# Performance work log

Hardware: AMD Instinct MI355X
Metric: run time of the kernel (lower is better)

The kernel has to match this reference:

```python
import jax, jax.numpy as jnp
import numpy as np

N_ATOMS = 10000
N_EDGES = 250000
F_DIM = 128
N_RBF = 20
CUTOFF = 5.0
N_INT = 3
EPS = 1e-8


def setup_inputs() -> dict:
    key = jax.random.key(0)
    ks = jax.random.split(key, 16)
    inp = {}
    inp["atomic_numbers"] = jax.random.randint(ks[0], (N_ATOMS,), 1, 101)
    # positions in a 5 Angstrom box so many pairs lie inside the cutoff
    inp["R"] = jax.random.uniform(ks[1], (N_ATOMS, 3), dtype=jnp.float32) * 5.0
    idx_i = jnp.sort(jax.random.randint(ks[2], (N_EDGES,), 0, N_ATOMS))
    # ensure idx_j != idx_i so d_ij > 0
    idx_j = (idx_i + 1 + jax.random.randint(ks[3], (N_EDGES,), 0, N_ATOMS - 1)) % N_ATOMS
    inp["idx_i"] = idx_i
    inp["idx_j"] = idx_j
    inp["offsets"] = jnp.zeros((N_EDGES, 3), dtype=jnp.float32)

    def w(k, shape):
        fan_in = shape[-2]
        return jax.random.normal(k, shape, dtype=jnp.float32) / np.sqrt(fan_in).astype(np.float32)

    inp["emb"] = jax.random.normal(ks[4], (101, F_DIM), dtype=jnp.float32)
    inp["filt_W"] = w(ks[5], (N_RBF, 3 * F_DIM))
    inp["filt_b"] = jax.random.normal(ks[6], (3 * F_DIM,), dtype=jnp.float32) * 0.01
    inp["int_W1"] = w(ks[7], (N_INT, F_DIM, F_DIM))
    inp["int_b1"] = jnp.zeros((N_INT, 1, F_DIM), dtype=jnp.float32)
    inp["int_W2"] = w(ks[8], (N_INT, F_DIM, 3 * F_DIM))
    inp["int_b2"] = jnp.zeros((N_INT, 1, 3 * F_DIM), dtype=jnp.float32)
    inp["mix_Wmu"] = w(ks[9], (N_INT, F_DIM, 2 * F_DIM))
    inp["mix_W1"] = w(ks[10], (N_INT, 2 * F_DIM, F_DIM))
    inp["mix_b1"] = jnp.zeros((N_INT, 1, F_DIM), dtype=jnp.float32)
    inp["mix_W2"] = w(ks[11], (N_INT, F_DIM, 3 * F_DIM))
    inp["mix_b2"] = jnp.zeros((N_INT, 1, 3 * F_DIM), dtype=jnp.float32)
    return inp


def painn_forward(atomic_numbers, idx_i, idx_j, R, offsets, emb, filt_W, filt_b,
                  int_W1, int_b1, int_W2, int_b2,
                  mix_Wmu, mix_W1, mix_b1, mix_W2, mix_b2):
    n_atoms = atomic_numbers.shape[0]
    # geometry
    r_ij = R[idx_j] - R[idx_i] + offsets                      # [E,3]
    d_ij = jnp.linalg.norm(r_ij, axis=1, keepdims=True)       # [E,1]
    dir_ij = r_ij / d_ij                                      # [E,3]
    # Gaussian radial basis + cosine cutoff (schnetpack defaults)
    centers = jnp.linspace(0.0, CUTOFF, N_RBF, dtype=jnp.float32)
    coeff = -0.5 / (centers[1] - centers[0]) ** 2
    phi = jnp.exp(coeff * (d_ij[..., None] - centers) ** 2)   # [E,1,N_RBF]
    fcut = 0.5 * (jnp.cos(d_ij * (jnp.pi / CUTOFF)) + 1.0) * (d_ij < CUTOFF)  # [E,1]
    Wij = (phi @ filt_W + filt_b) * fcut[..., None]           # [E,1,3F] (shared filters)

    q = emb[atomic_numbers][:, None, :]                       # [N,1,F]
    mu = jnp.zeros((n_atoms, 3, F_DIM), dtype=q.dtype)        # [N,3,F]

    for i in range(N_INT):
        # ---- interaction (equivariant message passing) ----
        x = jax.nn.silu(q @ int_W1[i] + int_b1[i]) @ int_W2[i] + int_b2[i]  # [N,1,3F]
        xj = x[idx_j]                                          # [E,1,3F]
        muj = mu[idx_j]                                        # [E,3,F]
        xw = Wij * xj                                          # [E,1,3F]
        dq, dmuR, dmumu = jnp.split(xw, 3, axis=-1)            # each [E,1,F]
        dq = jax.ops.segment_sum(dq, idx_i, num_segments=n_atoms)          # [N,1,F]
        dmu = dmuR * dir_ij[..., None] + dmumu * muj           # [E,3,F]
        dmu = jax.ops.segment_sum(dmu, idx_i, num_segments=n_atoms)        # [N,3,F]
        q = q + dq
        mu = mu + dmu
        # ---- mixing (intra-atomic) ----
        mu_mix = mu @ mix_Wmu[i]                               # [N,3,2F]
        mu_V, mu_W = jnp.split(mu_mix, 2, axis=-1)             # [N,3,F] each
        mu_Vn = jnp.sqrt(jnp.sum(mu_V ** 2, axis=-2, keepdims=True) + EPS)  # [N,1,F]
        ctx = jnp.concatenate([q, mu_Vn], axis=-1)             # [N,1,2F]
        xm = jax.nn.silu(ctx @ mix_W1[i] + mix_b1[i]) @ mix_W2[i] + mix_b2[i]  # [N,1,3F]
        dq_intra, dmu_intra, dqmu_intra = jnp.split(xm, 3, axis=-1)
        dmu_intra = dmu_intra * mu_W                           # [N,3,F]
        dqmu_intra = dqmu_intra * jnp.sum(mu_V * mu_W, axis=1, keepdims=True)  # [N,1,F]
        q = q + dq_intra + dqmu_intra
        mu = mu + dmu_intra

    return q.squeeze(1), mu                                    # [N,F], [N,3,F]


def reference(atomic_numbers, R, idx_i, idx_j, offsets, emb, filt_W, filt_b,
              int_W1, int_b1, int_W2, int_b2,
              mix_Wmu, mix_W1, mix_b1, mix_W2, mix_b2):
    return painn_forward(atomic_numbers, idx_i, idx_j, R, offsets, emb, filt_W, filt_b,
                         int_W1, int_b1, int_W2, int_b2,
                         mix_Wmu, mix_W1, mix_b1, mix_W2, mix_b2)
```

## Files before the change

kernel.cpp:

```cpp
#include <hip/hip_runtime.h>
#include <math.h>

#define NA 10000
#define NE 250000
#define FD 128
#define NRBF 20
#define RCUT 5.0f

typedef _Float16 h16;
typedef __attribute__((ext_vector_type(8))) _Float16 half8;
typedef __attribute__((ext_vector_type(4))) float f32x4;

static __device__ __forceinline__ half8 f32x8_to_h8(const float* p) {
    float4 a = *(const float4*)p;
    float4 b = *(const float4*)(p + 4);
    half8 r;
    r[0] = (h16)a.x; r[1] = (h16)a.y; r[2] = (h16)a.z; r[3] = (h16)a.w;
    r[4] = (h16)b.x; r[5] = (h16)b.y; r[6] = (h16)b.z; r[7] = (h16)b.w;
    return r;
}
static __device__ __forceinline__ float silu(float v) {
    return v / (1.f + expf(-v));
}

__global__ __launch_bounds__(256) void setup_kernel(
    const float* __restrict__ R, const int* __restrict__ idx_i,
    const int* __restrict__ idx_j, const float* __restrict__ offsets,
    float* __restrict__ dir, h16* __restrict__ ph, int* __restrict__ row_start,
    const float* __restrict__ int_W1, const float* __restrict__ int_W2,
    const float* __restrict__ mix_Wmu, const float* __restrict__ mix_W1,
    const float* __restrict__ mix_W2,
    h16* __restrict__ W1t, h16* __restrict__ W2t, h16* __restrict__ WmuT,
    h16* __restrict__ mW1t, h16* __restrict__ mW2t,
    const float* __restrict__ filt_W, const float* __restrict__ filt_b,
    h16* __restrict__ fwt)
{
    const int b = blockIdx.x;
    if (b < 977) {
        int e = b * 256 + threadIdx.x;
        if (e >= NE) return;
        int i = idx_i[e], j = idx_j[e];
        float rx = R[j * 3 + 0] - R[i * 3 + 0] + offsets[e * 3 + 0];
        float ry = R[j * 3 + 1] - R[i * 3 + 1] + offsets[e * 3 + 1];
        float rz = R[j * 3 + 2] - R[i * 3 + 2] + offsets[e * 3 + 2];
        float d = sqrtf(rx * rx + ry * ry + rz * rz);
        float inv = 1.f / d;
        float fcut = 0.f;
        if (d < RCUT) fcut = 0.5f * (cosf(d * (3.14159265358979323846f / RCUT)) + 1.f);
        *(float4*)&dir[(size_t)e * 4] = make_float4(rx * inv, ry * inv, rz * inv, 0.f);
        h16* pp = ph + (size_t)e * 32;
        const float delta = RCUT / 19.f;
        const float coeff = -0.5f / (delta * delta);
#pragma unroll
        for (int r = 0; r < NRBF; ++r) {
            float dc = d - (float)r * delta;
            pp[r] = (h16)(expf(coeff * dc * dc) * fcut);
        }
        pp[20] = (h16)fcut;
#pragma unroll
        for (int r = 21; r < 32; ++r) pp[r] = (h16)0.f;
    } else if (b < 1017) {
        int n = (b - 977) * 256 + threadIdx.x;
        if (n > NA) return;
        int lo = 0, hi = NE;
        while (lo < hi) {
            int mid = (lo + hi) >> 1;
            if (idx_i[mid] < n) lo = mid + 1; else hi = mid;
        }
        row_start[n] = lo;
    } else {
        int idx = (b - 1017) * 256 + threadIdx.x;
        if (idx < 49152) {
            int bt = idx >> 14, rem = idx & 16383;
            int nn = rem >> 7, kk = rem & 127;
            W1t[idx] = (h16)int_W1[(size_t)bt * 16384 + kk * 128 + nn];
        } else if ((idx -= 49152) < 147456) {
            int bt = idx / 49152, rem = idx - bt * 49152;
            int nn = rem >> 7, kk = rem & 127;
            W2t[idx] = (h16)int_W2[(size_t)bt * 49152 + kk * 384 + nn];
        } else if ((idx -= 147456) < 98304) {
            int bt = idx >> 15, rem = idx & 32767;
            int nn = rem >> 7, kk = rem & 127;
            WmuT[idx] = (h16)mix_Wmu[(size_t)bt * 32768 + kk * 256 + nn];
        } else if ((idx -= 98304) < 98304) {
            int bt = idx >> 15, rem = idx & 32767;
            int nn = rem >> 8, kk = rem & 255;
            mW1t[idx] = (h16)mix_W1[(size_t)bt * 32768 + kk * 128 + nn];
        } else if ((idx -= 98304) < 147456) {
            int bt = idx / 49152, rem = idx - bt * 49152;
            int nn = rem >> 7, kk = rem & 127;
            mW2t[idx] = (h16)mix_W2[(size_t)bt * 49152 + kk * 384 + nn];
        } else if ((idx -= 147456) < 12288) {
            int nn = idx >> 5, kk = idx & 31;
            float v = 0.f;
            if (kk < 20) v = filt_W[kk * 384 + nn];
            else if (kk == 20) v = filt_b[nn];
            fwt[idx] = (h16)v;
        }
    }
}

__global__ __launch_bounds__(256) void intmlp0_kernel(
    const int* __restrict__ Z, const float* __restrict__ emb, float* __restrict__ q,
    const h16* __restrict__ W1t, const float* __restrict__ b1,
    const h16* __restrict__ W2t, const float* __restrict__ b2, h16* __restrict__ x16)
{
    __shared__ h16 Hs[16 * 136];
    const int tid = threadIdx.x;
    const int wave = tid >> 6, lane = tid & 63;
    const int ar = lane & 15, kg = lane >> 4;
    const size_t row0 = (size_t)blockIdx.x * 16;

    {
        int a = tid >> 4, f0 = (tid & 15) * 8;
        const float* src = emb + (size_t)Z[row0 + a] * 128 + f0;
        float4 v0 = *(const float4*)src;
        float4 v1 = *(const float4*)(src + 4);
        *(float4*)&q[(row0 + a) * 128 + f0] = v0;
        *(float4*)&q[(row0 + a) * 128 + f0 + 4] = v1;
    }
    const int zr = Z[row0 + ar];
    f32x4 a1[2] = {};
    for (int ks = 0; ks < 128; ks += 32) {
        int k = ks + kg * 8;
        half8 af = f32x8_to_h8(emb + (size_t)zr * 128 + k);
#pragma unroll
        for (int tt = 0; tt < 2; ++tt) {
            int t = wave * 2 + tt;
            half8 bf = *(const half8*)&W1t[(size_t)(t * 16 + ar) * 128 + k];
            a1[tt] = __builtin_amdgcn_mfma_f32_16x16x32_f16(af, bf, a1[tt], 0, 0, 0);
        }
    }
#pragma unroll
    for (int tt = 0; tt < 2; ++tt) {
        int col = (wave * 2 + tt) * 16 + ar;
        float bb = b1[col];
#pragma unroll
        for (int r = 0; r < 4; ++r)
            Hs[(kg * 4 + r) * 136 + col] = (h16)silu(a1[tt][r] + bb);
    }
    __syncthreads();
    f32x4 a2[6] = {};
    for (int ks = 0; ks < 128; ks += 32) {
        int k = ks + kg * 8;
        half8 af = *(const half8*)&Hs[ar * 136 + k];
#pragma unroll
        for (int tt = 0; tt < 6; ++tt) {
            int t = wave * 6 + tt;
            half8 bf = *(const half8*)&W2t[(size_t)(t * 16 + ar) * 128 + k];
            a2[tt] = __builtin_amdgcn_mfma_f32_16x16x32_f16(af, bf, a2[tt], 0, 0, 0);
        }
    }
#pragma unroll
    for (int tt = 0; tt < 6; ++tt) {
        int col = (wave * 6 + tt) * 16 + ar;
        float bb = b2[col];
#pragma unroll
        for (int r = 0; r < 4; ++r)
            x16[(row0 + kg * 4 + r) * 384 + col] = (h16)(a2[tt][r] + bb);
    }
}

template<bool HAS_MU>
__global__ __launch_bounds__(128) void edge_kernel(
    const float* __restrict__ dir, const h16* __restrict__ ph,
    const h16* __restrict__ fwt,
    const int* __restrict__ row_start, const int* __restrict__ idx_j,
    const h16* __restrict__ x16, const h16* __restrict__ mu16p,
    const float* __restrict__ mup, float* __restrict__ mun,
    h16* __restrict__ mu16n, float* __restrict__ q)
{
    const int n = blockIdx.x, tid = threadIdx.x;
    const int wave = tid >> 6, lane = tid & 63;
    const int c = lane & 15, kg = lane >> 4;
    const int e0 = row_start[n], e1 = row_start[n + 1];

    float adq[4] = {}, am0[4] = {}, am1[4] = {}, am2[4] = {};

    for (int eg = e0; eg < e1; eg += 16) {
        int ea = eg + c; if (ea >= e1) ea = e1 - 1;
        half8 af = *(const half8*)&ph[(size_t)ea * 32 + kg * 8];
        f32x4 cw0[4], cw1[4], cw2[4];
#pragma unroll
        for (int tf = 0; tf < 4; ++tf) {
            f32x4 z = {0.f, 0.f, 0.f, 0.f};
            half8 b0 = *(const half8*)&fwt[(size_t)(((4 * wave + tf) * 16 + c)) * 32 + kg * 8];
            cw0[tf] = __builtin_amdgcn_mfma_f32_16x16x32_f16(af, b0, z, 0, 0, 0);
            half8 b1 = *(const half8*)&fwt[(size_t)(((8 + 4 * wave + tf) * 16 + c)) * 32 + kg * 8];
            cw1[tf] = __builtin_amdgcn_mfma_f32_16x16x32_f16(af, b1, z, 0, 0, 0);
            if (HAS_MU) {
                half8 b2 = *(const half8*)&fwt[(size_t)(((16 + 4 * wave + tf) * 16 + c)) * 32 + kg * 8];
                cw2[tf] = __builtin_amdgcn_mfma_f32_16x16x32_f16(af, b2, z, 0, 0, 0);
            } else {
                cw2[tf] = z;
            }
        }
#pragma unroll
        for (int r = 0; r < 4; ++r) {
            int e = eg + kg * 4 + r;
            if (e < e1) {
                int j = idx_j[e];
                float4 g = *(const float4*)&dir[(size_t)e * 4];
                const h16* xb = x16 + (size_t)j * 384;
#pragma unroll
                for (int tf = 0; tf < 4; ++tf) {
                    int fo = wave * 64 + tf * 16 + c;
                    float x0 = (float)xb[fo];
                    float x1 = (float)xb[128 + fo];
                    adq[tf] = fmaf(cw0[tf][r], x0, adq[tf]);
                    float t1 = cw1[tf][r] * x1;
                    if (HAS_MU) {
                        const h16* mb = mu16p + (size_t)j * 384;
                        float x2 = (float)xb[256 + fo];
                        float t2 = cw2[tf][r] * x2;
                        am0[tf] += t1 * g.x + t2 * (float)mb[fo];
                        am1[tf] += t1 * g.y + t2 * (float)mb[128 + fo];
                        am2[tf] += t1 * g.z + t2 * (float)mb[256 + fo];
                    } else {
                        am0[tf] = fmaf(t1, g.x, am0[tf]);
                        am1[tf] = fmaf(t1, g.y, am1[tf]);
                        am2[tf] = fmaf(t1, g.z, am2[tf]);
                    }
                }
            }
        }
    }

#pragma unroll
    for (int tf = 0; tf < 4; ++tf) {
        adq[tf] += __shfl_xor(adq[tf], 16); adq[tf] += __shfl_xor(adq[tf], 32);
        am0[tf] += __shfl_xor(am0[tf], 16); am0[tf] += __shfl_xor(am0[tf], 32);
        am1[tf] += __shfl_xor(am1[tf], 16); am1[tf] += __shfl_xor(am1[tf], 32);
        am2[tf] += __shfl_xor(am2[tf], 16); am2[tf] += __shfl_xor(am2[tf], 32);
    }
    if (kg == 0) {
        size_t b = (size_t)n * 384;
#pragma unroll
        for (int tf = 0; tf < 4; ++tf) {
            int fo = wave * 64 + tf * 16 + c;
            q[(size_t)n * 128 + fo] += adq[tf];
            float m0 = (HAS_MU ? mup[b + fo] : 0.f) + am0[tf];
            float m1 = (HAS_MU ? mup[b + 128 + fo] : 0.f) + am1[tf];
            float m2 = (HAS_MU ? mup[b + 256 + fo] : 0.f) + am2[tf];
            mun[b + fo] = m0; mun[b + 128 + fo] = m1; mun[b + 256 + fo] = m2;
            mu16n[b + fo] = (h16)m0; mu16n[b + 128 + fo] = (h16)m1; mu16n[b + 256 + fo] = (h16)m2;
        }
    }
}

__global__ __launch_bounds__(256) void mixint_kernel(
    const h16* __restrict__ mu16n, const h16* __restrict__ WmuT,
    const h16* __restrict__ W1t, const float* __restrict__ b1,
    const h16* __restrict__ W2t, const float* __restrict__ b2,
    float* __restrict__ q, float* __restrict__ mu, h16* __restrict__ mu16w,
    const h16* __restrict__ nW1t, const float* __restrict__ nb1,
    const h16* __restrict__ nW2t, const float* __restrict__ nb2,
    h16* __restrict__ x16)
{
    __shared__ h16 MM[48 * 264];
    __shared__ h16 CT[16 * 264];
    __shared__ h16 Hs[16 * 136];
    __shared__ h16 XM[16 * 392];
    const int tid = threadIdx.x;
    const int wave = tid >> 6, lane = tid & 63;
    const int ar = lane & 15, kg = lane >> 4;
    const size_t row0 = (size_t)blockIdx.x * 16;

    {
        f32x4 acc[3][4] = {};
        int aloc[3], dloc[3];
#pragma unroll
        for (int rt = 0; rt < 3; ++rt) {
            int rr = rt * 16 + ar;
            aloc[rt] = rr / 3;
            dloc[rt] = rr - 3 * aloc[rt];
        }
        for (int ks = 0; ks < 128; ks += 32) {
            int k = ks + kg * 8;
            half8 afr[3];
#pragma unroll
            for (int rt = 0; rt < 3; ++rt)
                afr[rt] = *(const half8*)&mu16n[(row0 + aloc[rt]) * 384 + dloc[rt] * 128 + k];
#pragma unroll
            for (int ct = 0; ct < 4; ++ct) {
                int cc = wave * 4 + ct;
                half8 bf = *(const half8*)&WmuT[(size_t)(cc * 16 + ar) * 128 + k];
#pragma unroll
                for (int rt = 0; rt < 3; ++rt)
                    acc[rt][ct] = __builtin_amdgcn_mfma_f32_16x16x32_f16(afr[rt], bf, acc[rt][ct], 0, 0, 0);
            }
        }
#pragma unroll
        for (int rt = 0; rt < 3; ++rt)
#pragma unroll
            for (int ct = 0; ct < 4; ++ct) {
                int col = (wave * 4 + ct) * 16 + ar;
#pragma unroll
                for (int r = 0; r < 4; ++r)
                    MM[(rt * 16 + kg * 4 + r) * 264 + col] = (h16)acc[rt][ct][r];
            }
    }
    __syncthreads();

    {
        int a = tid >> 4, fi = (tid & 15) * 8;
        const float* qp = q + (row0 + a) * 128 + fi;
        float4 q0 = *(const float4*)qp;
        float4 q1 = *(const float4*)(qp + 4);
        float qv[8] = {q0.x, q0.y, q0.z, q0.w, q1.x, q1.y, q1.z, q1.w};
#pragma unroll
        for (int jj = 0; jj < 8; ++jj) {
            int ff = fi + jj;
            float v0 = (float)MM[(a * 3 + 0) * 264 + ff];
            float v1 = (float)MM[(a * 3 + 1) * 264 + ff];
            float v2 = (float)MM[(a * 3 + 2) * 264 + ff];
            CT[a * 264 + 128 + ff] = (h16)sqrtf(v0 * v0 + v1 * v1 + v2 * v2 + 1e-8f);
            CT[a * 264 + ff] = (h16)qv[jj];
        }
    }
    __syncthreads();

    {
        f32x4 a1[2] = {};
        for (int ks = 0; ks < 256; ks += 32) {
            int k = ks + kg * 8;
            half8 af = *(const half8*)&CT[ar * 264 + k];
#pragma unroll
            for (int tt = 0; tt < 2; ++tt) {
                int t = wave * 2 + tt;
                half8 bf = *(const half8*)&W1t[(size_t)(t * 16 + ar) * 256 + k];
                a1[tt] = __builtin_amdgcn_mfma_f32_16x16x32_f16(af, bf, a1[tt], 0, 0, 0);
            }
        }
#pragma unroll
        for (int tt = 0; tt < 2; ++tt) {
            int col = (wave * 2 + tt) * 16 + ar;
            float bb = b1[col];
#pragma unroll
            for (int r = 0; r < 4; ++r)
                Hs[(kg * 4 + r) * 136 + col] = (h16)silu(a1[tt][r] + bb);
        }
    }
    __syncthreads();

    {
        f32x4 a2[6] = {};
        for (int ks = 0; ks < 128; ks += 32) {
            int k = ks + kg * 8;
            half8 af = *(const half8*)&Hs[ar * 136 + k];
#pragma unroll
            for (int tt = 0; tt < 6; ++tt) {
                int t = wave * 6 + tt;
                half8 bf = *(const half8*)&W2t[(size_t)(t * 16 + ar) * 128 + k];
                a2[tt] = __builtin_amdgcn_mfma_f32_16x16x32_f16(af, bf, a2[tt], 0, 0, 0);
            }
        }
#pragma unroll
        for (int tt = 0; tt < 6; ++tt) {
            int col = (wave * 6 + tt) * 16 + ar;
            float bb = b2[col];
#pragma unroll
            for (int r = 0; r < 4; ++r)
                XM[(kg * 4 + r) * 392 + col] = (h16)(a2[tt][r] + bb);
        }
    }
    __syncthreads();

    {
        int a = tid >> 4, fi = (tid & 15) * 8;
        size_t n = row0 + a;
#pragma unroll
        for (int jj = 0; jj < 8; ++jj) {
            int ff = fi + jj;
            float dq  = (float)XM[a * 392 + ff];
            float dm  = (float)XM[a * 392 + 128 + ff];
            float dqm = (float)XM[a * 392 + 256 + ff];
            float v0 = (float)MM[(a * 3 + 0) * 264 + ff], w0 = (float)MM[(a * 3 + 0) * 264 + 128 + ff];
            float v1 = (float)MM[(a * 3 + 1) * 264 + ff], w1 = (float)MM[(a * 3 + 1) * 264 + 128 + ff];
            float v2 = (float)MM[(a * 3 + 2) * 264 + ff], w2 = (float)MM[(a * 3 + 2) * 264 + 128 + ff];
            float sv = v0 * w0 + v1 * w1 + v2 * w2;
            float qn = q[n * 128 + ff] + dq + dqm * sv;
            q[n * 128 + ff] = qn;
            CT[a * 264 + ff] = (h16)qn;
            size_t b = n * 384 + ff;
            float m0 = mu[b] + dm * w0;
            float m1 = mu[b + 128] + dm * w1;
            float m2 = mu[b + 256] + dm * w2;
            mu[b] = m0; mu[b + 128] = m1; mu[b + 256] = m2;
            mu16w[b] = (h16)m0; mu16w[b + 128] = (h16)m1; mu16w[b + 256] = (h16)m2;
        }
    }
    if (!nW1t) return;
    __syncthreads();

    {
        f32x4 a1[2] = {};
        for (int ks = 0; ks < 128; ks += 32) {
            int k = ks + kg * 8;
            half8 af = *(const half8*)&CT[ar * 264 + k];
#pragma unroll
            for (int tt = 0; tt < 2; ++tt) {
                int t = wave * 2 + tt;
                half8 bf = *(const half8*)&nW1t[(size_t)(t * 16 + ar) * 128 + k];
                a1[tt] = __builtin_amdgcn_mfma_f32_16x16x32_f16(af, bf, a1[tt], 0, 0, 0);
            }
        }
#pragma unroll
        for (int tt = 0; tt < 2; ++tt) {
            int col = (wave * 2 + tt) * 16 + ar;
            float bb = nb1[col];
#pragma unroll
            for (int r = 0; r < 4; ++r)
                Hs[(kg * 4 + r) * 136 + col] = (h16)silu(a1[tt][r] + bb);
        }
        __syncthreads();
        f32x4 a2[6] = {};
        for (int ks = 0; ks < 128; ks += 32) {
            int k = ks + kg * 8;
            half8 af = *(const half8*)&Hs[ar * 136 + k];
#pragma unroll
            for (int tt = 0; tt < 6; ++tt) {
                int t = wave * 6 + tt;
                half8 bf = *(const half8*)&nW2t[(size_t)(t * 16 + ar) * 128 + k];
                a2[tt] = __builtin_amdgcn_mfma_f32_16x16x32_f16(af, bf, a2[tt], 0, 0, 0);
            }
        }
#pragma unroll
        for (int tt = 0; tt < 6; ++tt) {
            int col = (wave * 6 + tt) * 16 + ar;
            float bb = nb2[col];
#pragma unroll
            for (int r = 0; r < 4; ++r)
                x16[(row0 + kg * 4 + r) * 384 + col] = (h16)(a2[tt][r] + bb);
        }
    }
}

extern "C" void kernel_launch(void* const* d_in, const int* in_sizes, int n_in,
                              void* d_out, int out_size, void* d_ws, size_t ws_size,
                              hipStream_t stream)
{
    const int*   Z       = (const int*)d_in[0];
    const float* R       = (const float*)d_in[1];
    const int*   idx_i   = (const int*)d_in[2];
    const int*   idx_j   = (const int*)d_in[3];
    const float* offsets = (const float*)d_in[4];
    const float* emb     = (const float*)d_in[5];
    const float* filt_W  = (const float*)d_in[6];
    const float* filt_b  = (const float*)d_in[7];
    const float* int_W1  = (const float*)d_in[8];
    const float* int_b1  = (const float*)d_in[9];
    const float* int_W2  = (const float*)d_in[10];
    const float* int_b2  = (const float*)d_in[11];
    const float* mix_Wmu = (const float*)d_in[12];
    const float* mix_W1  = (const float*)d_in[13];
    const float* mix_b1  = (const float*)d_in[14];
    const float* mix_W2  = (const float*)d_in[15];
    const float* mix_b2  = (const float*)d_in[16];

    float* q_out  = (float*)d_out;
    float* mu_out = (float*)d_out + (size_t)NA * FD;

    char* base = (char*)d_ws;
    size_t o = 0;
    auto alloc = [&](size_t bytes) -> void* {
        void* p = base + o;
        o += (bytes + 255) & ~(size_t)255;
        return p;
    };
    float* dir    = (float*)alloc((size_t)NE * 4 * 4);
    h16*   ph     = (h16*)alloc((size_t)NE * 32 * 2);
    h16*   x16    = (h16*)alloc((size_t)NA * 384 * 2);
    h16*   mu16a  = (h16*)alloc((size_t)NA * 384 * 2);
    h16*   mu16b  = (h16*)alloc((size_t)NA * 384 * 2);
    float* mu_ws  = (float*)alloc((size_t)NA * 384 * 4);
    h16*   W1t    = (h16*)alloc((size_t)3 * 128 * 128 * 2);
    h16*   W2t    = (h16*)alloc((size_t)3 * 384 * 128 * 2);
    h16*   WmuT   = (h16*)alloc((size_t)3 * 256 * 128 * 2);
    h16*   mW1t   = (h16*)alloc((size_t)3 * 128 * 256 * 2);
    h16*   mW2t   = (h16*)alloc((size_t)3 * 384 * 128 * 2);
    h16*   fwt    = (h16*)alloc((size_t)384 * 32 * 2);
    int*   row_st = (int*)alloc((size_t)(NA + 1) * 4);

    setup_kernel<<<3177, 256, 0, stream>>>(R, idx_i, idx_j, offsets, dir, ph, row_st,
                                           int_W1, int_W2, mix_Wmu, mix_W1, mix_W2,
                                           W1t, W2t, WmuT, mW1t, mW2t,
                                           filt_W, filt_b, fwt);

    intmlp0_kernel<<<NA / 16, 256, 0, stream>>>(Z, emb, q_out,
                                                W1t, int_b1, W2t, int_b2, x16);
    edge_kernel<false><<<NA, 128, 0, stream>>>(dir, ph, fwt, row_st, idx_j,
                                               x16, nullptr, nullptr, mu_out, mu16b, q_out);
    mixint_kernel<<<NA / 16, 256, 0, stream>>>(
        mu16b, WmuT, mW1t, mix_b1, mW2t, mix_b2, q_out, mu_out, mu16b,
        W1t + 16384, int_b1 + 128, W2t + 49152, int_b2 + 384, x16);

    edge_kernel<true><<<NA, 128, 0, stream>>>(dir, ph, fwt, row_st, idx_j,
                                              x16, mu16b, mu_out, mu_ws, mu16a, q_out);
    mixint_kernel<<<NA / 16, 256, 0, stream>>>(
        mu16a, WmuT + 32768, mW1t + 32768, mix_b1 + 128, mW2t + 49152, mix_b2 + 384,
        q_out, mu_ws, mu16a,
        W1t + 32768, int_b1 + 256, W2t + 98304, int_b2 + 768, x16);

    edge_kernel<true><<<NA, 128, 0, stream>>>(dir, ph, fwt, row_st, idx_j,
                                              x16, mu16a, mu_ws, mu_out, mu16b, q_out);
    mixint_kernel<<<NA / 16, 256, 0, stream>>>(
        mu16b, WmuT + 65536, mW1t + 65536, mix_b1 + 256, mW2t + 98304, mix_b2 + 768,
        q_out, mu_out, mu16b,
        nullptr, nullptr, nullptr, nullptr, nullptr);
}
```

Baseline: 474.9 us.

## Transpose edge MFMA so lanes own edges and gather contiguous half4 features

The edge kernel now uses four waves per atom, each owning 32 features. The filter weights become the register-resident A operand, loaded once per block, and the per-edge RBF values become the B operand. Each lane now handles one edge and four consecutive features, so gathers from x16 and mu16 become vectorized half4 loads instead of scalar half loads. The next edge group's ph, idx_j and dir are prefetched one iteration ahead. The cost is a longer 4-step shuffle reduction across the 16 edge lanes, and 256-thread blocks that may lower occupancy.

```diff
diff --git a/kernel.cpp b/kernel.cpp
--- a/kernel.cpp
+++ b/kernel.cpp
@@ -9,6 +9,7 @@
 
 typedef _Float16 h16;
 typedef __attribute__((ext_vector_type(8))) _Float16 half8;
+typedef __attribute__((ext_vector_type(4))) _Float16 half4;
 typedef __attribute__((ext_vector_type(4))) float f32x4;
 
 static __device__ __forceinline__ half8 f32x8_to_h8(const float* p) {
@@ -162,7 +163,7 @@
 }
 
 template<bool HAS_MU>
-__global__ __launch_bounds__(128) void edge_kernel(
+__global__ __launch_bounds__(256) void edge_kernel(
     const float* __restrict__ dir, const h16* __restrict__ ph,
     const h16* __restrict__ fwt,
     const int* __restrict__ row_start, const int* __restrict__ idx_j,
@@ -174,52 +175,74 @@
     const int wave = tid >> 6, lane = tid & 63;
     const int c = lane & 15, kg = lane >> 4;
     const int e0 = row_start[n], e1 = row_start[n + 1];
-
-    float adq[4] = {}, am0[4] = {}, am1[4] = {}, am2[4] = {};
-
-    for (int eg = e0; eg < e1; eg += 16) {
-        int ea = eg + c; if (ea >= e1) ea = e1 - 1;
-        half8 af = *(const half8*)&ph[(size_t)ea * 32 + kg * 8];
-        f32x4 cw0[4], cw1[4], cw2[4];
-#pragma unroll
-        for (int tf = 0; tf < 4; ++tf) {
+    const int f0 = wave * 32;
+
+    half8 afq[2], afr[2], afm[2];
+#pragma unroll
+    for (int t = 0; t < 2; ++t) {
+        int fr = f0 + 16 * t + c;
+        afq[t] = *(const half8*)&fwt[(size_t)fr * 32 + kg * 8];
+        afr[t] = *(const half8*)&fwt[(size_t)(128 + fr) * 32 + kg * 8];
+        if (HAS_MU)
+            afm[t] = *(const half8*)&fwt[(size_t)(256 + fr) * 32 + kg * 8];
+    }
+
+    f32x4 adq[2] = {}, am0[2] = {}, am1[2] = {}, am2[2] = {};
+
+    if (e0 < e1) {
+        int ec = e0 + c; int ecl = ec < e1 ? ec : e1 - 1;
+        half8 bf = *(const half8*)&ph[(size_t)ecl * 32 + kg * 8];
+        int j = idx_j[ecl];
+        float4 g = *(const float4*)&dir[(size_t)ecl * 4];
+
+        for (int eg = e0; eg < e1; eg += 16) {
+            half8 bf_c = bf; int j_c = j; float4 g_c = g;
+            bool v_c = (eg + c) < e1;
+            int eg2 = eg + 16;
+            if (eg2 < e1) {
+                int e2 = eg2 + c; int ecl2 = e2 < e1 ? e2 : e1 - 1;
+                bf = *(const half8*)&ph[(size_t)ecl2 * 32 + kg * 8];
+                j = idx_j[ecl2];
+                g = *(const float4*)&dir[(size_t)ecl2 * 4];
+            }
             f32x4 z = {0.f, 0.f, 0.f, 0.f};
-            half8 b0 = *(const half8*)&fwt[(size_t)(((4 * wave + tf) * 16 + c)) * 32 + kg * 8];
-            cw0[tf] = __builtin_amdgcn_mfma_f32_16x16x32_f16(af, b0, z, 0, 0, 0);
-            half8 b1 = *(const half8*)&fwt[(size_t)(((8 + 4 * wave + tf) * 16 + c)) * 32 + kg * 8];
-            cw1[tf] = __builtin_amdgcn_mfma_f32_16x16x32_f16(af, b1, z, 0, 0, 0);
-            if (HAS_MU) {
-                half8 b2 = *(const half8*)&fwt[(size_t)(((16 + 4 * wave + tf) * 16 + c)) * 32 + kg * 8];
-                cw2[tf] = __builtin_amdgcn_mfma_f32_16x16x32_f16(af, b2, z, 0, 0, 0);
-            } else {
-                cw2[tf] = z;
-            }
-        }
-#pragma unroll
-        for (int r = 0; r < 4; ++r) {
-            int e = eg + kg * 4 + r;
-            if (e < e1) {
-                int j = idx_j[e];
-                float4 g = *(const float4*)&dir[(size_t)e * 4];
-                const h16* xb = x16 + (size_t)j * 384;
-#pragma unroll
-                for (int tf = 0; tf < 4; ++tf) {
-                    int fo = wave * 64 + tf * 16 + c;
-                    float x0 = (float)xb[fo];
-                    float x1 = (float)xb[128 + fo];
-                    adq[tf] = fmaf(cw0[tf][r], x0, adq[tf]);
-                    float t1 = cw1[tf][r] * x1;
+            f32x4 cwq[2], cwr[2], cwm[2];
+#pragma unroll
+            for (int t = 0; t < 2; ++t) {
+                cwq[t] = __builtin_amdgcn_mfma_f32_16x16x32_f16(afq[t], bf_c, z, 0, 0, 0);
+                cwr[t] = __builtin_amdgcn_mfma_f32_16x16x32_f16(afr[t], bf_c, z, 0, 0, 0);
+                if (HAS_MU)
+                    cwm[t] = __builtin_amdgcn_mfma_f32_16x16x32_f16(afm[t], bf_c, z, 0, 0, 0);
+            }
+            if (v_c) {
+                const h16* xb = x16 + (size_t)j_c * 384;
+#pragma unroll
+                for (int t = 0; t < 2; ++t) {
+                    int fb = f0 + 16 * t + kg * 4;
+                    half4 x0 = *(const half4*)&xb[fb];
+                    half4 x1 = *(const half4*)&xb[128 + fb];
+                    half4 x2, m0, m1, m2;
                     if (HAS_MU) {
-                        const h16* mb = mu16p + (size_t)j * 384;
-                        float x2 = (float)xb[256 + fo];
-                        float t2 = cw2[tf][r] * x2;
-                        am0[tf] += t1 * g.x + t2 * (float)mb[fo];
-                        am1[tf] += t1 * g.y + t2 * (float)mb[128 + fo];
-                        am2[tf] += t1 * g.z + t2 * (float)mb[256 + fo];
-                    } else {
-                        am0[tf] = fmaf(t1, g.x, am0[tf]);
-                        am1[tf] = fmaf(t1, g.y, am1[tf]);
-                        am2[tf] = fmaf(t1, g.z, am2[tf]);
+                        const h16* mb = mu16p + (size_t)j_c * 384;
+                        x2 = *(const half4*)&xb[256 + fb];
+                        m0 = *(const half4*)&mb[fb];
+                        m1 = *(const half4*)&mb[128 + fb];
+                        m2 = *(const half4*)&mb[256 + fb];
+                    }
+#pragma unroll
+                    for (int r = 0; r < 4; ++r) {
+                        adq[t][r] = fmaf(cwq[t][r], (float)x0[r], adq[t][r]);
+                        float t1 = cwr[t][r] * (float)x1[r];
+                        if (HAS_MU) {
+                            float t2 = cwm[t][r] * (float)x2[r];
+                            am0[t][r] += t1 * g_c.x + t2 * (float)m0[r];
+                            am1[t][r] += t1 * g_c.y + t2 * (float)m1[r];
+                            am2[t][r] += t1 * g_c.z + t2 * (float)m2[r];
+                        } else {
+                            am0[t][r] = fmaf(t1, g_c.x, am0[t][r]);
+                            am1[t][r] = fmaf(t1, g_c.y, am1[t][r]);
+                            am2[t][r] = fmaf(t1, g_c.z, am2[t][r]);
+                        }
                     }
                 }
             }
@@ -227,23 +250,48 @@
     }
 
 #pragma unroll
-    for (int tf = 0; tf < 4; ++tf) {
-        adq[tf] += __shfl_xor(adq[tf], 16); adq[tf] += __shfl_xor(adq[tf], 32);
-        am0[tf] += __shfl_xor(am0[tf], 16); am0[tf] += __shfl_xor(am0[tf], 32);
-        am1[tf] += __shfl_xor(am1[tf], 16); am1[tf] += __shfl_xor(am1[tf], 32);
-        am2[tf] += __shfl_xor(am2[tf], 16); am2[tf] += __shfl_xor(am2[tf], 32);
-    }
-    if (kg == 0) {
-        size_t b = (size_t)n * 384;
-#pragma unroll
-        for (int tf = 0; tf < 4; ++tf) {
-            int fo = wave * 64 + tf * 16 + c;
-            q[(size_t)n * 128 + fo] += adq[tf];
-            float m0 = (HAS_MU ? mup[b + fo] : 0.f) + am0[tf];
-            float m1 = (HAS_MU ? mup[b + 128 + fo] : 0.f) + am1[tf];
-            float m2 = (HAS_MU ? mup[b + 256 + fo] : 0.f) + am2[tf];
-            mun[b + fo] = m0; mun[b + 128 + fo] = m1; mun[b + 256 + fo] = m2;
-            mu16n[b + fo] = (h16)m0; mu16n[b + 128 + fo] = (h16)m1; mu16n[b + 256 + fo] = (h16)m2;
+    for (int t = 0; t < 2; ++t)
+#pragma unroll
+        for (int r = 0; r < 4; ++r) {
+            float a = adq[t][r], b0 = am0[t][r], b1 = am1[t][r], b2 = am2[t][r];
+#pragma unroll
+            for (int m = 1; m < 16; m <<= 1) {
+                a  += __shfl_xor(a, m);
+                b0 += __shfl_xor(b0, m);
+                b1 += __shfl_xor(b1, m);
+                b2 += __shfl_xor(b2, m);
+            }
+            adq[t][r] = a; am0[t][r] = b0; am1[t][r] = b1; am2[t][r] = b2;
+        }
+
+    if (c == 0) {
+        size_t nb = (size_t)n * 384;
+#pragma unroll
+        for (int t = 0; t < 2; ++t) {
+            int fb = f0 + 16 * t + kg * 4;
+            float4 qv = *(float4*)&q[(size_t)n * 128 + fb];
+            qv.x += adq[t][0]; qv.y += adq[t][1]; qv.z += adq[t][2]; qv.w += adq[t][3];
+            *(float4*)&q[(size_t)n * 128 + fb] = qv;
+            float4 p0, p1, p2;
+            if (HAS_MU) {
+                p0 = *(const float4*)&mup[nb + fb];
+                p1 = *(const float4*)&mup[nb + 128 + fb];
+                p2 = *(const float4*)&mup[nb + 256 + fb];
+            } else {
+                p0 = p1 = p2 = make_float4(0.f, 0.f, 0.f, 0.f);
+            }
+            p0.x += am0[t][0]; p0.y += am0[t][1]; p0.z += am0[t][2]; p0.w += am0[t][3];
+            p1.x += am1[t][0]; p1.y += am1[t][1]; p1.z += am1[t][2]; p1.w += am1[t][3];
+            p2.x += am2[t][0]; p2.y += am2[t][1]; p2.z += am2[t][2]; p2.w += am2[t][3];
+            *(float4*)&mun[nb + fb] = p0;
+            *(float4*)&mun[nb + 128 + fb] = p1;
+            *(float4*)&mun[nb + 256 + fb] = p2;
+            half4 h0 = {(h16)p0.x, (h16)p0.y, (h16)p0.z, (h16)p0.w};
+            half4 h1 = {(h16)p1.x, (h16)p1.y, (h16)p1.z, (h16)p1.w};
+            half4 h2 = {(h16)p2.x, (h16)p2.y, (h16)p2.z, (h16)p2.w};
+            *(half4*)&mu16n[nb + fb] = h0;
+            *(half4*)&mu16n[nb + 128 + fb] = h1;
+            *(half4*)&mu16n[nb + 256 + fb] = h2;
         }
     }
 }
@@ -489,20 +537,20 @@
 
     intmlp0_kernel<<<NA / 16, 256, 0, stream>>>(Z, emb, q_out,
                                                 W1t, int_b1, W2t, int_b2, x16);
-    edge_kernel<false><<<NA, 128, 0, stream>>>(dir, ph, fwt, row_st, idx_j,
+    edge_kernel<false><<<NA, 256, 0, stream>>>(dir, ph, fwt, row_st, idx_j,
                                                x16, nullptr, nullptr, mu_out, mu16b, q_out);
     mixint_kernel<<<NA / 16, 256, 0, stream>>>(
         mu16b, WmuT, mW1t, mix_b1, mW2t, mix_b2, q_out, mu_out, mu16b,
         W1t + 16384, int_b1 + 128, W2t + 49152, int_b2 + 384, x16);
 
-    edge_kernel<true><<<NA, 128, 0, stream>>>(dir, ph, fwt, row_st, idx_j,
+    edge_kernel<true><<<NA, 256, 0, stream>>>(dir, ph, fwt, row_st, idx_j,
                                               x16, mu16b, mu_out, mu_ws, mu16a, q_out);
     mixint_kernel<<<NA / 16, 256, 0, stream>>>(
         mu16a, WmuT + 32768, mW1t + 32768, mix_b1 + 128, mW2t + 49152, mix_b2 + 384,
         q_out, mu_ws, mu16a,
         W1t + 32768, int_b1 + 256, W2t + 98304, int_b2 + 768, x16);
 
-    edge_kernel<true><<<NA, 128, 0, stream>>>(dir, ph, fwt, row_st, idx_j,
+    edge_kernel<true><<<NA, 256, 0, stream>>>(dir, ph, fwt, row_st, idx_j,
                                               x16, mu16a, mu_ws, mu_out, mu16b, q_out);
     mixint_kernel<<<NA / 16, 256, 0, stream>>>(
         mu16b, WmuT + 65536, mW1t + 65536, mix_b1 + 256, mW2t + 98304, mix_b2 + 768,
```

New measurement: 570.2 us. +20.1%, slower.
